# Optimization experiments

Measured on AMD Instinct MI355X. Metric: run time of the kernel, lower is better.

## Reference

```python
import jax, jax.numpy as jnp
import numpy as np

MODEL_DIM = 1024
NUM_HEADS = 16
HEAD_DIM = MODEL_DIM // NUM_HEADS


def _rope(t):
    # t: [B, S, H, hd] -- ESM-style rotary (rotate_half on halves, freqs tiled)
    B, S, H, hd = t.shape
    inv_freq = 1.0 / (10000.0 ** (jnp.arange(0, hd, 2, dtype=jnp.float32) / hd))  # [hd/2]
    freqs = jnp.arange(S, dtype=jnp.float32)[:, None] * inv_freq[None, :]          # [S, hd/2]
    emb = jnp.concatenate([freqs, freqs], axis=-1)                                 # [S, hd]
    cos = jnp.cos(emb)[None, :, None, :].astype(t.dtype)
    sin = jnp.sin(emb)[None, :, None, :].astype(t.dtype)
    t1, t2 = jnp.split(t, 2, axis=-1)
    rot = jnp.concatenate([-t2, t1], axis=-1)
    return t * cos + rot * sin


def setup_inputs() -> dict:
    key = jax.random.key(0)
    ks = jax.random.split(key, 5)
    D = MODEL_DIM
    s = 1.0 / np.sqrt(D)
    return {
        "x": jax.random.normal(ks[0], (2, 2048, D), dtype=jnp.float32),
        "in_proj_w": jax.random.normal(ks[1], (3 * D, D), dtype=jnp.float32) * s,
        "in_proj_b": jax.random.normal(ks[2], (3 * D,), dtype=jnp.float32) * 0.02,
        "out_proj_w": jax.random.normal(ks[3], (D, D), dtype=jnp.float32) * s,
        "out_proj_b": jax.random.normal(ks[4], (D,), dtype=jnp.float32) * 0.02,
    }


def reference(x, in_proj_w, in_proj_b, out_proj_w, out_proj_b):
    B, S, D = x.shape
    H, hd = NUM_HEADS, HEAD_DIM
    # --- manual _in_proj using MHA's packed in_proj params ---
    combined = jnp.einsum('bsd,ed->bse', x, in_proj_w) + in_proj_b  # [B,S,3D]
    q0, k0, v0 = jnp.split(combined, 3, axis=-1)
    # --- rotary on q/k per head ---
    q1 = _rope(q0.reshape(B, S, H, hd)).reshape(B, S, D)
    k1 = _rope(k0.reshape(B, S, H, hd)).reshape(B, S, D)
    # --- nn.MultiheadAttention re-projects q/k/v with the SAME in_proj ---
    Wq, Wk, Wv = in_proj_w[:D], in_proj_w[D:2 * D], in_proj_w[2 * D:]
    bq, bk, bv = in_proj_b[:D], in_proj_b[D:2 * D], in_proj_b[2 * D:]
    q = (jnp.einsum('bsd,ed->bse', q1, Wq) + bq).reshape(B, S, H, hd)
    k = (jnp.einsum('bsd,ed->bse', k1, Wk) + bk).reshape(B, S, H, hd)
    v = (jnp.einsum('bsd,ed->bse', v0, Wv) + bv).reshape(B, S, H, hd)
    # --- scaled dot-product attention ---
    scale = 1.0 / np.sqrt(hd)
    scores = jnp.einsum('bqhd,bkhd->bhqk', q, k) * scale
    attn = jax.nn.softmax(scores, axis=-1)
    ctx = jnp.einsum('bhqk,bkhd->bqhd', attn, v).reshape(B, S, D)
    return jnp.einsum('bsd,ed->bse', ctx, out_proj_w) + out_proj_b
```

## Files before the change

kernel.cpp:

```cpp
#include <hip/hip_runtime.h>
#include <math.h>

#define D_MODEL   1024
#define N_HEADS   16
#define H_DIM     64
#define SEQ       2048
#define BATCH     2
#define ROWS      (BATCH * SEQ)
#define THREE_D   (3 * D_MODEL)

#define QK_SCALE  (0.125f * 1.44269504088896340736f)

typedef __attribute__((ext_vector_type(8))) short short8v;
typedef __attribute__((ext_vector_type(4))) float f32x4;
typedef __attribute__((ext_vector_type(4))) unsigned int uint4v;
typedef __attribute__((ext_vector_type(2))) unsigned int uint2v;

union Frag { uint4v u; short8v s; };

__device__ __forceinline__ void async_copy16(const void* g, void* l)
{
    __builtin_amdgcn_global_load_lds(
        (const __attribute__((address_space(1))) void*)g,
        (__attribute__((address_space(3))) void*)l,
        16, 0, 0);
}

__device__ __forceinline__ int swz8(int row, int oct)
{
    return oct ^ ((row ^ (row >> 2)) & 7);
}

__device__ __forceinline__ uint2v shfl_u2(uint2v v, int src)
{
    uint2v r;
    r.x = (unsigned)__shfl((int)v.x, src);
    r.y = (unsigned)__shfl((int)v.y, src);
    return r;
}

__device__ __forceinline__ void split2x8(const float* v, uint4v& U1, uint4v& U2)
{
    unsigned b1[8], b2[8];
#pragma unroll
    for (int j = 0; j < 8; ++j) {
        const unsigned u = __float_as_uint(v[j]);
        b1[j] = u;
        const float r = v[j] - __uint_as_float(u & 0xFFFF0000u);
        b2[j] = __float_as_uint(r);
    }
    U1 = (uint4v){ (b1[0]>>16)|(b1[1]&0xFFFF0000u), (b1[2]>>16)|(b1[3]&0xFFFF0000u),
                   (b1[4]>>16)|(b1[5]&0xFFFF0000u), (b1[6]>>16)|(b1[7]&0xFFFF0000u) };
    U2 = (uint4v){ (b2[0]>>16)|(b2[1]&0xFFFF0000u), (b2[2]>>16)|(b2[3]&0xFFFF0000u),
                   (b2[4]>>16)|(b2[5]&0xFFFF0000u), (b2[6]>>16)|(b2[7]&0xFFFF0000u) };
}

__device__ __forceinline__ void pack_store(unsigned short* rowp, int col, float val)
{
    unsigned short* d = rowp + ((col >> 5) << 6) + (col & 31);
    const unsigned u = __float_as_uint(val);
    d[0]  = (unsigned short)(u >> 16);
    const float r = val - __uint_as_float(u & 0xFFFF0000u);
    d[32] = (unsigned short)(__float_as_uint(r) >> 16);
}

__global__ __launch_bounds__(256)
void split_pack(const float* __restrict__ in, unsigned short* __restrict__ out)
{
    const size_t e0 = ((size_t)blockIdx.x * 256 + threadIdx.x) * 8;
    const float4 a0 = *reinterpret_cast<const float4*>(in + e0);
    const float4 a1 = *reinterpret_cast<const float4*>(in + e0 + 4);
    float v[8] = { a0.x, a0.y, a0.z, a0.w, a1.x, a1.y, a1.z, a1.w };
    uint4v U1, U2;
    split2x8(v, U1, U2);
    unsigned short* d = out + ((e0 >> 5) << 6) + (e0 & 31);
    *reinterpret_cast<uint4v*>(d)      = U1;
    *reinterpret_cast<uint4v*>(d + 32) = U2;
}

__global__ void rope_table(float* __restrict__ tab)
{
    const int idx = blockIdx.x * 256 + threadIdx.x;
    const int s = idx >> 5;
    const int i = idx & 31;
    const double inv = pow(10000.0, -(double)(2 * i) / 64.0);
    const double f = (double)s * inv;
    tab[idx * 2 + 0] = (float)cos(f);
    tab[idx * 2 + 1] = (float)sin(f);
}

__global__ __launch_bounds__(256, 2)
void gemm_p(const unsigned short* __restrict__ Ap, int ldA2,
            const unsigned short* __restrict__ Bp, int ldB2,
            const float* __restrict__ bias,
            float* __restrict__ C, int ldc, int K,
            int nbx, size_t segA, size_t segB, int segBias, size_t segC)
{
    __shared__ __align__(16) unsigned short As[2][128 * 64];
    __shared__ __align__(16) unsigned short Bs[2][128 * 64];

    const int fid  = blockIdx.y * gridDim.x + blockIdx.x;
    const int bxpx = gridDim.x >> 3;
    const int xcd  = fid & 7;
    const int idx  = fid >> 3;
    const int bxx  = xcd * bxpx + idx % bxpx;
    const int by   = idx / bxpx;

    const int seg = bxx / nbx;
    const int bxs = bxx - seg * nbx;
    const int bm  = by * 128;
    const int bn  = bxs * 128;
    Ap   += (size_t)seg * segA;
    Bp   += (size_t)seg * segB;
    bias += seg * segBias;
    C    += (size_t)seg * segC;

    const int t    = threadIdx.x;
    const int wid  = t >> 6;
    const int lane = t & 63;
    const int wr   = wid >> 1;
    const int wc   = wid & 1;
    const int cl   = lane & 15;
    const int kq   = lane >> 4;
    const int lrow = lane >> 3;
    const int gs   = lane & 7;

    auto stage = [&](int buf, int k0) {
        const int gl = gs ^ lrow;
#pragma unroll
        for (int q = 0; q < 4; ++q) {
            const int r0  = (wid * 4 + q) * 8;
            const int row = r0 + lrow;
            async_copy16(Ap + (size_t)(bm + row) * ldA2 + (k0 << 1) + (gl << 3),
                         &As[buf][r0 * 64]);
            async_copy16(Bp + (size_t)(bn + row) * ldB2 + (k0 << 1) + (gl << 3),
                         &Bs[buf][r0 * 64]);
        }
    };

    f32x4 acc[4][4];
#pragma unroll
    for (int m = 0; m < 4; ++m)
#pragma unroll
        for (int n = 0; n < 4; ++n) acc[m][n] = (f32x4)(0.f);

    const int NT = K >> 5;
    stage(0, 0);

    for (int it = 0; it < NT; ++it) {
        __syncthreads();
        if (it + 1 < NT)
            stage((it + 1) & 1, (it + 1) << 5);

        const unsigned short* as = As[it & 1];
        const unsigned short* bs = Bs[it & 1];

        short8v A1[4], A2[4], B1[4], B2[4];
#pragma unroll
        for (int m = 0; m < 4; ++m) {
            const int r = wr * 64 + m * 16 + cl;
            const unsigned short* ar = as + r * 64;
            A1[m] = *reinterpret_cast<const short8v*>(ar + (( kq      ^ (r & 7)) << 3));
            A2[m] = *reinterpret_cast<const short8v*>(ar + (((kq + 4) ^ (r & 7)) << 3));
        }
#pragma unroll
        for (int n = 0; n < 4; ++n) {
            const int r = wc * 64 + n * 16 + cl;
            const unsigned short* br = bs + r * 64;
            B1[n] = *reinterpret_cast<const short8v*>(br + (( kq      ^ (r & 7)) << 3));
            B2[n] = *reinterpret_cast<const short8v*>(br + (((kq + 4) ^ (r & 7)) << 3));
        }

#pragma unroll
        for (int m = 0; m < 4; ++m)
#pragma unroll
            for (int n = 0; n < 4; ++n) {
                f32x4 c = acc[m][n];
                c = __builtin_amdgcn_mfma_f32_16x16x32_bf16(A1[m], B1[n], c, 0, 0, 0);
                c = __builtin_amdgcn_mfma_f32_16x16x32_bf16(A2[m], B1[n], c, 0, 0, 0);
                c = __builtin_amdgcn_mfma_f32_16x16x32_bf16(A1[m], B2[n], c, 0, 0, 0);
                acc[m][n] = c;
            }
    }

    const int rw = lane >> 4;
#pragma unroll
    for (int n = 0; n < 4; ++n) {
        const int col = bn + wc * 64 + n * 16 + cl;
        const float bv = bias[col];
#pragma unroll
        for (int m = 0; m < 4; ++m) {
            const size_t rbase = (size_t)(bm + wr * 64 + m * 16 + rw * 4);
#pragma unroll
            for (int i = 0; i < 4; ++i)
                C[(rbase + i) * ldc + col] = acc[m][n][i] + bv;
        }
    }
}

__global__ __launch_bounds__(256, 2)
void gemm_p_pack(const unsigned short* __restrict__ Ap, int ldA2,
                 const unsigned short* __restrict__ Bp, int ldB2,
                 const float* __restrict__ bias,
                 unsigned short* __restrict__ Cp, int ldc2, int K,
                 int nbx, size_t segA, size_t segB, int segBias, size_t segC)
{
    __shared__ __align__(16) unsigned short As[2][128 * 64];
    __shared__ __align__(16) unsigned short Bs[2][128 * 64];

    const int fid  = blockIdx.y * gridDim.x + blockIdx.x;
    const int bxpx = gridDim.x >> 3;
    const int xcd  = fid & 7;
    const int idx  = fid >> 3;
    const int bxx  = xcd * bxpx + idx % bxpx;
    const int by   = idx / bxpx;

    const int seg = bxx / nbx;
    const int bxs = bxx - seg * nbx;
    const int bm  = by * 128;
    const int bn  = bxs * 128;
    Ap   += (size_t)seg * segA;
    Bp   += (size_t)seg * segB;
    bias += seg * segBias;
    Cp   += (size_t)seg * segC;

    const int t    = threadIdx.x;
    const int wid  = t >> 6;
    const int lane = t & 63;
    const int wr   = wid >> 1;
    const int wc   = wid & 1;
    const int cl   = lane & 15;
    const int kq   = lane >> 4;
    const int lrow = lane >> 3;
    const int gs   = lane & 7;

    auto stage = [&](int buf, int k0) {
        const int gl = gs ^ lrow;
#pragma unroll
        for (int q = 0; q < 4; ++q) {
            const int r0  = (wid * 4 + q) * 8;
            const int row = r0 + lrow;
            async_copy16(Ap + (size_t)(bm + row) * ldA2 + (k0 << 1) + (gl << 3),
                         &As[buf][r0 * 64]);
            async_copy16(Bp + (size_t)(bn + row) * ldB2 + (k0 << 1) + (gl << 3),
                         &Bs[buf][r0 * 64]);
        }
    };

    f32x4 acc[4][4];
#pragma unroll
    for (int m = 0; m < 4; ++m)
#pragma unroll
        for (int n = 0; n < 4; ++n) acc[m][n] = (f32x4)(0.f);

    const int NT = K >> 5;
    stage(0, 0);

    for (int it = 0; it < NT; ++it) {
        __syncthreads();
        if (it + 1 < NT)
            stage((it + 1) & 1, (it + 1) << 5);

        const unsigned short* as = As[it & 1];
        const unsigned short* bs = Bs[it & 1];

        short8v A1[4], A2[4], B1[4], B2[4];
#pragma unroll
        for (int m = 0; m < 4; ++m) {
            const int r = wr * 64 + m * 16 + cl;
            const unsigned short* ar = as + r * 64;
            A1[m] = *reinterpret_cast<const short8v*>(ar + (( kq      ^ (r & 7)) << 3));
            A2[m] = *reinterpret_cast<const short8v*>(ar + (((kq + 4) ^ (r & 7)) << 3));
        }
#pragma unroll
        for (int n = 0; n < 4; ++n) {
            const int r = wc * 64 + n * 16 + cl;
            const unsigned short* br = bs + r * 64;
            B1[n] = *reinterpret_cast<const short8v*>(br + (( kq      ^ (r & 7)) << 3));
            B2[n] = *reinterpret_cast<const short8v*>(br + (((kq + 4) ^ (r & 7)) << 3));
        }

#pragma unroll
        for (int m = 0; m < 4; ++m)
#pragma unroll
            for (int n = 0; n < 4; ++n) {
                f32x4 c = acc[m][n];
                c = __builtin_amdgcn_mfma_f32_16x16x32_bf16(A1[m], B1[n], c, 0, 0, 0);
                c = __builtin_amdgcn_mfma_f32_16x16x32_bf16(A2[m], B1[n], c, 0, 0, 0);
                c = __builtin_amdgcn_mfma_f32_16x16x32_bf16(A1[m], B2[n], c, 0, 0, 0);
                acc[m][n] = c;
            }
    }

    const int rw = lane >> 4;
#pragma unroll
    for (int n = 0; n < 4; ++n) {
        const int col = bn + wc * 64 + n * 16 + cl;
        const float bv = bias[col];
#pragma unroll
        for (int m = 0; m < 4; ++m) {
            const size_t rbase = (size_t)(bm + wr * 64 + m * 16 + rw * 4);
#pragma unroll
            for (int i = 0; i < 4; ++i)
                pack_store(Cp + (rbase + i) * (size_t)ldc2, col, acc[m][n][i] + bv);
        }
    }
}

__global__ __launch_bounds__(256, 2)
void gemm_p_rope(const unsigned short* __restrict__ Ap, int ldA2,
                 const unsigned short* __restrict__ Bp, int ldB2,
                 const float* __restrict__ bias,
                 const float* __restrict__ tab,
                 unsigned short* __restrict__ out, int K)
{
    __shared__ __align__(16) unsigned short As[2][128 * 64];
    __shared__ __align__(16) unsigned short Bs[2][128 * 64];

    const int fid  = blockIdx.y * gridDim.x + blockIdx.x;
    const int bxpx = gridDim.x >> 3;
    const int xcd  = fid & 7;
    const int idx  = fid >> 3;
    const int bxx  = xcd * bxpx + idx % bxpx;
    const int by   = idx / bxpx;

    const int bm  = by * 128;
    const int bn  = bxx * 128;

    const int t    = threadIdx.x;
    const int wid  = t >> 6;
    const int lane = t & 63;
    const int wr   = wid >> 1;
    const int wc   = wid & 1;
    const int cl   = lane & 15;
    const int kq   = lane >> 4;
    const int lrow = lane >> 3;
    const int gs   = lane & 7;

    auto stage = [&](int buf, int k0) {
        const int gl = gs ^ lrow;
#pragma unroll
        for (int q = 0; q < 4; ++q) {
            const int r0  = (wid * 4 + q) * 8;
            const int row = r0 + lrow;
            async_copy16(Ap + (size_t)(bm + row) * ldA2 + (k0 << 1) + (gl << 3),
                         &As[buf][r0 * 64]);
            async_copy16(Bp + (size_t)(bn + row) * ldB2 + (k0 << 1) + (gl << 3),
                         &Bs[buf][r0 * 64]);
        }
    };

    f32x4 acc[4][4];
#pragma unroll
    for (int m = 0; m < 4; ++m)
#pragma unroll
        for (int n = 0; n < 4; ++n) acc[m][n] = (f32x4)(0.f);

    const int NT = K >> 5;
    stage(0, 0);

    for (int it = 0; it < NT; ++it) {
        __syncthreads();
        if (it + 1 < NT)
            stage((it + 1) & 1, (it + 1) << 5);

        const unsigned short* as = As[it & 1];
        const unsigned short* bs = Bs[it & 1];

        short8v A1[4], A2[4], B1[4], B2[4];
#pragma unroll
        for (int m = 0; m < 4; ++m) {
            const int r = wr * 64 + m * 16 + cl;
            const unsigned short* ar = as + r * 64;
            A1[m] = *reinterpret_cast<const short8v*>(ar + (( kq      ^ (r & 7)) << 3));
            A2[m] = *reinterpret_cast<const short8v*>(ar + (((kq + 4) ^ (r & 7)) << 3));
        }
#pragma unroll
        for (int n = 0; n < 4; ++n) {
            const int r = wc * 64 + n * 16 + cl;
            const unsigned short* br = bs + r * 64;
            B1[n] = *reinterpret_cast<const short8v*>(br + (( kq      ^ (r & 7)) << 3));
            B2[n] = *reinterpret_cast<const short8v*>(br + (((kq + 4) ^ (r & 7)) << 3));
        }

#pragma unroll
        for (int m = 0; m < 4; ++m)
#pragma unroll
            for (int n = 0; n < 4; ++n) {
                f32x4 c = acc[m][n];
                c = __builtin_amdgcn_mfma_f32_16x16x32_bf16(A1[m], B1[n], c, 0, 0, 0);
                c = __builtin_amdgcn_mfma_f32_16x16x32_bf16(A2[m], B1[n], c, 0, 0, 0);
                c = __builtin_amdgcn_mfma_f32_16x16x32_bf16(A1[m], B2[n], c, 0, 0, 0);
                acc[m][n] = c;
            }
    }

    const int rw = lane >> 4;
    const bool doRope = (bn < 2 * D_MODEL);
#pragma unroll
    for (int n = 0; n < 2; ++n) {
        const int colA = bn + wc * 64 + n * 16 + cl;
        const int colB = colA + 32;
        const float bvA = bias[colA];
        const float bvB = bias[colB];
        const int d = n * 16 + cl;
#pragma unroll
        for (int m = 0; m < 4; ++m) {
            const size_t rbase = (size_t)(bm + wr * 64 + m * 16 + rw * 4);
#pragma unroll
            for (int i = 0; i < 4; ++i) {
                const size_t row = rbase + i;
                const float t1 = acc[m][n][i]     + bvA;
                const float t2 = acc[m][n + 2][i] + bvB;
                float r1 = t1, r2 = t2;
                if (doRope) {
                    const int s = (int)(row & (SEQ - 1));
                    const float c  = tab[(s * 32 + d) * 2 + 0];
                    const float sn = tab[(s * 32 + d) * 2 + 1];
                    r1 = t1 * c - t2 * sn;
                    r2 = t2 * c + t1 * sn;
                }
                unsigned short* op = out + row * (size_t)(THREE_D * 2);
                pack_store(op, colA, r1);
                pack_store(op, colB, r2);
            }
        }
    }
}

__global__ __launch_bounds__(512)
void attn_mfma(const unsigned short* __restrict__ Qp,
               const unsigned short* __restrict__ Kp,
               const unsigned short* __restrict__ Vp,
               unsigned short* __restrict__ pctx)
{
    __shared__ __align__(16) short Ks1[2][64 * 64];
    __shared__ __align__(16) short Ks2[2][64 * 64];
    __shared__ __align__(16) short Vt1[2][64 * 64];
    __shared__ __align__(16) short Vt2[2][64 * 64];

    const int fid = blockIdx.y * gridDim.x + blockIdx.x;
    const int bh  = (fid & 7) * 4 + ((fid >> 3) & 3);
    const int q0  = (fid >> 5) * 128;
    const int b   = bh >> 4;
    const int h   = bh & 15;
    const size_t rowBase = (size_t)b * SEQ;
    const int hs = h * H_DIM * 2;

    const int t    = threadIdx.x;
    const int w    = t >> 6;
    const int lane = t & 63;
    const int cl   = lane & 15;
    const int g    = lane >> 4;
    const int g2   = g >> 1;
    const int srcA = cl + 32 * (g & 1);
    const int srcB = srcA + 16;

    const int krow = t >> 2;
    const int dob  = (t & 3) * 2;
    const int t2   = t - 256;
    const int vkq  = t2 >> 4;
    const int vdq  = t2 & 15;

    const int ksrc = (dob >> 2) * 64 + (dob & 3) * 8;

    Frag qf[2][2];
    {
        const unsigned short* qp =
            Qp + (rowBase + q0 + w * 16 + cl) * (size_t)(D_MODEL * 2) + hs;
#pragma unroll
        for (int c = 0; c < 2; ++c) {
            qf[c][0].u = *reinterpret_cast<const uint4v*>(qp + c * 64 + g * 8);
            qf[c][1].u = *reinterpret_cast<const uint4v*>(qp + c * 64 + 32 + g * 8);
        }
    }

    f32x4 acc[4];
#pragma unroll
    for (int s = 0; s < 4; ++s) acc[s] = (f32x4)(0.f);
    float m = -1e30f;
    float l = 0.f;

    uint4v k1a, k1b, k2a, k2b;
    uint2v vp1[4], vp2[4];

    auto load_tile = [&](int k0) {
        if (w < 4) {
            const unsigned short* kp =
                Kp + (rowBase + k0 + krow) * (size_t)(D_MODEL * 2) + hs + ksrc;
            k1a = *reinterpret_cast<const uint4v*>(kp);
            k1b = *reinterpret_cast<const uint4v*>(kp + 8);
            k2a = *reinterpret_cast<const uint4v*>(kp + 32);
            k2b = *reinterpret_cast<const uint4v*>(kp + 40);
        } else {
            const unsigned short* vrow =
                Vp + (rowBase + k0 + vkq * 4) * (size_t)(D_MODEL * 2) + hs
                + (((vdq * 4) >> 5) << 6) + ((vdq * 4) & 31);
#pragma unroll
            for (int r = 0; r < 4; ++r) {
                vp1[r] = *reinterpret_cast<const uint2v*>(vrow + r * (D_MODEL * 2));
                vp2[r] = *reinterpret_cast<const uint2v*>(vrow + r * (D_MODEL * 2) + 32);
            }
        }
    };

    auto write_tile = [&](int buf) {
        if (w < 4) {
            short* kb1 = Ks1[buf] + krow * 64;
            short* kb2 = Ks2[buf] + krow * 64;
            *reinterpret_cast<uint4v*>(kb1 + swz8(krow, dob    ) * 8) = k1a;
            *reinterpret_cast<uint4v*>(kb1 + swz8(krow, dob + 1) * 8) = k1b;
            *reinterpret_cast<uint4v*>(kb2 + swz8(krow, dob    ) * 8) = k2a;
            *reinterpret_cast<uint4v*>(kb2 + swz8(krow, dob + 1) * 8) = k2b;
        } else {
            const int lo = vkq >> 1;
            const int hf = (vkq & 1) * 4;
#pragma unroll
            for (int rr = 0; rr < 4; ++rr) {
                const int row  = 4 * vdq + rr;
                const int word = rr >> 1;
                const int sh   = (rr & 1) * 16;
                const unsigned e10 = (vp1[0][word] >> sh) & 0xFFFFu;
                const unsigned e11 = (vp1[1][word] >> sh) & 0xFFFFu;
                const unsigned e12 = (vp1[2][word] >> sh) & 0xFFFFu;
                const unsigned e13 = (vp1[3][word] >> sh) & 0xFFFFu;
                const unsigned e20 = (vp2[0][word] >> sh) & 0xFFFFu;
                const unsigned e21 = (vp2[1][word] >> sh) & 0xFFFFu;
                const unsigned e22 = (vp2[2][word] >> sh) & 0xFFFFu;
                const unsigned e23 = (vp2[3][word] >> sh) & 0xFFFFu;
                uint2v w1, w2;
                w1.x = e10 | (e11 << 16);
                w1.y = e12 | (e13 << 16);
                w2.x = e20 | (e21 << 16);
                w2.y = e22 | (e23 << 16);
                const int o = row * 64 + swz8(row, lo) * 8 + hf;
                *reinterpret_cast<uint2v*>(&Vt1[buf][o]) = w1;
                *reinterpret_cast<uint2v*>(&Vt2[buf][o]) = w2;
            }
        }
    };

    const int NT = SEQ / 64;

    load_tile(0);
    write_tile(0);

    for (int it = 0; it < NT; ++it) {
        __syncthreads();
        const int bf = it & 1;
        if (it + 1 < NT)
            load_tile((it + 1) * 64);

        f32x4 sacc[4];
#pragma unroll
        for (int ks = 0; ks < 4; ++ks) sacc[ks] = (f32x4)(0.f);

#pragma unroll
        for (int ks = 0; ks < 4; ++ks)
#pragma unroll
            for (int c = 0; c < 2; ++c) {
                const int row = ks * 16 + cl;
                const int po  = row * 64 + swz8(row, 4 * c + g) * 8;
                Frag ka1, ka2;
                ka1.s = *reinterpret_cast<const short8v*>(&Ks1[bf][po]);
                ka2.s = *reinterpret_cast<const short8v*>(&Ks2[bf][po]);
                f32x4 s = sacc[ks];
                s = __builtin_amdgcn_mfma_f32_16x16x32_bf16(ka1.s, qf[c][0].s, s, 0, 0, 0);
                s = __builtin_amdgcn_mfma_f32_16x16x32_bf16(ka2.s, qf[c][0].s, s, 0, 0, 0);
                s = __builtin_amdgcn_mfma_f32_16x16x32_bf16(ka1.s, qf[c][1].s, s, 0, 0, 0);
                sacc[ks] = s;
            }

        float tm = -1e30f;
#pragma unroll
        for (int ks = 0; ks < 4; ++ks)
#pragma unroll
            for (int i = 0; i < 4; ++i) tm = fmaxf(tm, sacc[ks][i]);
        tm = fmaxf(tm, __shfl_xor(tm, 16));
        tm = fmaxf(tm, __shfl_xor(tm, 32));

        const float mn = fmaxf(m, tm);
        const float sc = __builtin_amdgcn_exp2f((m - mn) * QK_SCALE);
        m = mn;
        const float mns = mn * QK_SCALE;

        float rs = 0.f;
        uint2v P1[4];
#pragma unroll
        for (int ks = 0; ks < 4; ++ks) {
            float p[4];
            unsigned ub[4];
#pragma unroll
            for (int i = 0; i < 4; ++i) {
                p[i] = __builtin_amdgcn_exp2f(fmaf(sacc[ks][i], QK_SCALE, -mns));
                rs += p[i];
                ub[i] = __float_as_uint(p[i]);
            }
            P1[ks] = (uint2v){ (ub[0] >> 16) | (ub[1] & 0xFFFF0000u),
                               (ub[2] >> 16) | (ub[3] & 0xFFFF0000u) };
        }
        rs += __shfl_xor(rs, 16);
        rs += __shfl_xor(rs, 32);
        l = l * sc + rs;

        float scv[4];
#pragma unroll
        for (int i = 0; i < 4; ++i) scv[i] = __shfl(sc, 4 * g + i);
#pragma unroll
        for (int s = 0; s < 4; ++s)
#pragma unroll
            for (int i = 0; i < 4; ++i) acc[s][i] *= scv[i];

#pragma unroll
        for (int c = 0; c < 2; ++c) {
            uint2v a0 = shfl_u2(P1[2 * c],     srcA);
            uint2v a1 = shfl_u2(P1[2 * c + 1], srcA);
            uint2v b0 = shfl_u2(P1[2 * c],     srcB);
            uint2v b1 = shfl_u2(P1[2 * c + 1], srcB);
            uint2v lo = g2 ? a1 : a0;
            uint2v hi = g2 ? b1 : b0;
            Frag pa;
            pa.u = (uint4v){ lo.x, lo.y, hi.x, hi.y };
#pragma unroll
            for (int s = 0; s < 4; ++s) {
                const int row = s * 16 + cl;
                const int vo  = row * 64 + swz8(row, 4 * c + g) * 8;
                Frag vb1, vb2;
                vb1.s = *reinterpret_cast<const short8v*>(&Vt1[bf][vo]);
                vb2.s = *reinterpret_cast<const short8v*>(&Vt2[bf][vo]);
                f32x4 a = acc[s];
                a = __builtin_amdgcn_mfma_f32_16x16x32_bf16(pa.s, vb1.s, a, 0, 0, 0);
                a = __builtin_amdgcn_mfma_f32_16x16x32_bf16(pa.s, vb2.s, a, 0, 0, 0);
                acc[s] = a;
            }
        }

        if (it + 1 < NT)
            write_tile(bf ^ 1);
    }

    const float inv = 1.f / l;
    float iv[4];
#pragma unroll
    for (int i = 0; i < 4; ++i) iv[i] = __shfl(inv, 4 * g + i);
#pragma unroll
    for (int s = 0; s < 4; ++s)
#pragma unroll
        for (int i = 0; i < 4; ++i) {
            const float val = acc[s][i] * iv[i];
            const size_t grow = rowBase + q0 + w * 16 + 4 * g + i;
            const int gc = h * H_DIM + s * 16 + cl;
            pack_store(pctx + grow * (size_t)(D_MODEL * 2), gc, val);
        }
}

extern "C" void kernel_launch(void* const* d_in, const int* in_sizes, int n_in,
                              void* d_out, int out_size, void* d_ws, size_t ws_size,
                              hipStream_t stream)
{
    const float* x    = (const float*)d_in[0];
    const float* Win  = (const float*)d_in[1];
    const float* bin  = (const float*)d_in[2];
    const float* Wout = (const float*)d_in[3];
    const float* bout = (const float*)d_in[4];
    float* out = (float*)d_out;

    float* R1 = (float*)d_ws;
    float* R2 = R1 + (size_t)ROWS * THREE_D;
    unsigned short* pW  = (unsigned short*)(R2 + (size_t)ROWS * THREE_D);
    unsigned short* pWo = pW + (size_t)THREE_D * D_MODEL * 2;
    float* tab = (float*)(pWo + (size_t)D_MODEL * D_MODEL * 2);

    unsigned short* px    = (unsigned short*)R1;
    unsigned short* qkvp  = (unsigned short*)R1;
    unsigned short* pcomb = (unsigned short*)R2;
    unsigned short* pctx  = (unsigned short*)R2;

    unsigned short* Qp = qkvp;
    unsigned short* Kp = qkvp + (size_t)ROWS * D_MODEL * 2;
    unsigned short* Vp = Kp  + (size_t)ROWS * D_MODEL * 2;

    const dim3 blk(256);

    rope_table<<<dim3(SEQ * 32 / 256), blk, 0, stream>>>(tab);

    split_pack<<<dim3(ROWS * D_MODEL / 8 / 256), blk, 0, stream>>>(x, px);
    split_pack<<<dim3(THREE_D * D_MODEL / 8 / 256), blk, 0, stream>>>(Win, pW);
    split_pack<<<dim3(D_MODEL * D_MODEL / 8 / 256), blk, 0, stream>>>(Wout, pWo);

    gemm_p_rope<<<dim3(24, 32), blk, 0, stream>>>(
        px, D_MODEL * 2, pW, D_MODEL * 2, bin, tab, pcomb, D_MODEL);

    gemm_p_pack<<<dim3(24, 32), blk, 0, stream>>>(
        pcomb, THREE_D * 2, pW, D_MODEL * 2, bin, qkvp, D_MODEL * 2, D_MODEL,
        8, (size_t)(D_MODEL * 2), (size_t)D_MODEL * D_MODEL * 2, D_MODEL,
        (size_t)ROWS * D_MODEL * 2);

    attn_mfma<<<dim3(SEQ / 128, BATCH * N_HEADS), dim3(512), 0, stream>>>(
        Qp, Kp, Vp, pctx);

    gemm_p<<<dim3(8, 32), blk, 0, stream>>>(
        pctx, D_MODEL * 2, pWo, D_MODEL * 2, bout, out, D_MODEL, D_MODEL,
        8, (size_t)0, (size_t)0, 0, (size_t)0);
}
```

Before: 347.1 us.

## Drop K low-part split in QK^T, add lazy softmax rescale, merge pack kernels

The attention QK^T product now uses only the high bf16 part of K and skips the K low-part MFMA, its LDS buffer and its global loads. This lowers precision compared with the previous split-bf16 scheme. The online softmax rescale now runs only when some lane's tile max exceeds the running max by more than a threshold, which removes per-tile exp and accumulator scaling. The three split_pack launches are merged into one kernel to cut launch overhead.

```diff
diff --git a/kernel.cpp b/kernel.cpp
--- a/kernel.cpp
+++ b/kernel.cpp
@@ -10,6 +10,7 @@
 #define THREE_D   (3 * D_MODEL)
 
 #define QK_SCALE  (0.125f * 1.44269504088896340736f)
+#define THR_RAW   (8.0f / QK_SCALE)
 
 typedef __attribute__((ext_vector_type(8))) short short8v;
 typedef __attribute__((ext_vector_type(4))) float f32x4;
@@ -65,9 +66,19 @@
 }
 
 __global__ __launch_bounds__(256)
-void split_pack(const float* __restrict__ in, unsigned short* __restrict__ out)
-{
-    const size_t e0 = ((size_t)blockIdx.x * 256 + threadIdx.x) * 8;
+void split_pack3(const float* __restrict__ x,    unsigned short* __restrict__ px,
+                 const float* __restrict__ w1,   unsigned short* __restrict__ pw1,
+                 const float* __restrict__ w2,   unsigned short* __restrict__ pw2)
+{
+    const int bid = blockIdx.x;
+    const float* in;
+    unsigned short* out;
+    size_t base;
+    if (bid < 2048)      { in = x;  out = px;  base = (size_t)bid * 2048; }
+    else if (bid < 3584) { in = w1; out = pw1; base = (size_t)(bid - 2048) * 2048; }
+    else                 { in = w2; out = pw2; base = (size_t)(bid - 3584) * 2048; }
+
+    const size_t e0 = base + (size_t)threadIdx.x * 8;
     const float4 a0 = *reinterpret_cast<const float4*>(in + e0);
     const float4 a1 = *reinterpret_cast<const float4*>(in + e0 + 4);
     float v[8] = { a0.x, a0.y, a0.z, a0.w, a1.x, a1.y, a1.z, a1.w };
@@ -435,7 +446,6 @@
                unsigned short* __restrict__ pctx)
 {
     __shared__ __align__(16) short Ks1[2][64 * 64];
-    __shared__ __align__(16) short Ks2[2][64 * 64];
     __shared__ __align__(16) short Vt1[2][64 * 64];
     __shared__ __align__(16) short Vt2[2][64 * 64];
 
@@ -481,7 +491,7 @@
     float m = -1e30f;
     float l = 0.f;
 
-    uint4v k1a, k1b, k2a, k2b;
+    uint4v k1a, k1b;
     uint2v vp1[4], vp2[4];
 
     auto load_tile = [&](int k0) {
@@ -490,8 +500,6 @@
                 Kp + (rowBase + k0 + krow) * (size_t)(D_MODEL * 2) + hs + ksrc;
             k1a = *reinterpret_cast<const uint4v*>(kp);
             k1b = *reinterpret_cast<const uint4v*>(kp + 8);
-            k2a = *reinterpret_cast<const uint4v*>(kp + 32);
-            k2b = *reinterpret_cast<const uint4v*>(kp + 40);
         } else {
             const unsigned short* vrow =
                 Vp + (rowBase + k0 + vkq * 4) * (size_t)(D_MODEL * 2) + hs
@@ -507,11 +515,8 @@
     auto write_tile = [&](int buf) {
         if (w < 4) {
             short* kb1 = Ks1[buf] + krow * 64;
-            short* kb2 = Ks2[buf] + krow * 64;
             *reinterpret_cast<uint4v*>(kb1 + swz8(krow, dob    ) * 8) = k1a;
             *reinterpret_cast<uint4v*>(kb1 + swz8(krow, dob + 1) * 8) = k1b;
-            *reinterpret_cast<uint4v*>(kb2 + swz8(krow, dob    ) * 8) = k2a;
-            *reinterpret_cast<uint4v*>(kb2 + swz8(krow, dob + 1) * 8) = k2b;
         } else {
             const int lo = vkq >> 1;
             const int hf = (vkq & 1) * 4;
@@ -561,12 +566,10 @@
             for (int c = 0; c < 2; ++c) {
                 const int row = ks * 16 + cl;
                 const int po  = row * 64 + swz8(row, 4 * c + g) * 8;
-                Frag ka1, ka2;
+                Frag ka1;
                 ka1.s = *reinterpret_cast<const short8v*>(&Ks1[bf][po]);
-                ka2.s = *reinterpret_cast<const short8v*>(&Ks2[bf][po]);
                 f32x4 s = sacc[ks];
                 s = __builtin_amdgcn_mfma_f32_16x16x32_bf16(ka1.s, qf[c][0].s, s, 0, 0, 0);
-                s = __builtin_amdgcn_mfma_f32_16x16x32_bf16(ka2.s, qf[c][0].s, s, 0, 0, 0);
                 s = __builtin_amdgcn_mfma_f32_16x16x32_bf16(ka1.s, qf[c][1].s, s, 0, 0, 0);
                 sacc[ks] = s;
             }
@@ -579,10 +582,21 @@
         tm = fmaxf(tm, __shfl_xor(tm, 16));
         tm = fmaxf(tm, __shfl_xor(tm, 32));
 
-        const float mn = fmaxf(m, tm);
-        const float sc = __builtin_amdgcn_exp2f((m - mn) * QK_SCALE);
-        m = mn;
-        const float mns = mn * QK_SCALE;
+        const bool need = !__all(tm <= m + THR_RAW);
+        if (need) {
+            const float mn = fmaxf(m, tm);
+            const float sc = __builtin_amdgcn_exp2f((m - mn) * QK_SCALE);
+            m = mn;
+            l *= sc;
+            float scv[4];
+#pragma unroll
+            for (int i = 0; i < 4; ++i) scv[i] = __shfl(sc, 4 * g + i);
+#pragma unroll
+            for (int s = 0; s < 4; ++s)
+#pragma unroll
+                for (int i = 0; i < 4; ++i) acc[s][i] *= scv[i];
+        }
+        const float mns = m * QK_SCALE;
 
         float rs = 0.f;
         uint2v P1[4];
@@ -601,15 +615,7 @@
         }
         rs += __shfl_xor(rs, 16);
         rs += __shfl_xor(rs, 32);
-        l = l * sc + rs;
-
-        float scv[4];
-#pragma unroll
-        for (int i = 0; i < 4; ++i) scv[i] = __shfl(sc, 4 * g + i);
-#pragma unroll
-        for (int s = 0; s < 4; ++s)
-#pragma unroll
-            for (int i = 0; i < 4; ++i) acc[s][i] *= scv[i];
+        l += rs;
 
 #pragma unroll
         for (int c = 0; c < 2; ++c) {
@@ -684,9 +690,7 @@
 
     rope_table<<<dim3(SEQ * 32 / 256), blk, 0, stream>>>(tab);
 
-    split_pack<<<dim3(ROWS * D_MODEL / 8 / 256), blk, 0, stream>>>(x, px);
-    split_pack<<<dim3(THREE_D * D_MODEL / 8 / 256), blk, 0, stream>>>(Win, pW);
-    split_pack<<<dim3(D_MODEL * D_MODEL / 8 / 256), blk, 0, stream>>>(Wout, pWo);
+    split_pack3<<<dim3(4096), blk, 0, stream>>>(x, px, Win, pW, Wout, pWo);
 
     gemm_p_rope<<<dim3(24, 32), blk, 0, stream>>>(
         px, D_MODEL * 2, pW, D_MODEL * 2, bin, tab, pcomb, D_MODEL);
```

Result: faster. 324.9 us (-6.4%).
